# Performance work log

Measured on AMD Instinct MI355X. Metric: run time of the kernel, lower is better.

## Reference

```python
import jax, jax.numpy as jnp
import numpy as np

N_NODES = 50000
N_EDGES = 1600000
D = 128
LEAKY_SLOPE = 0.01  # torch nn.LeakyReLU default


def setup_inputs() -> dict:
    key = jax.random.key(0)
    ks = jax.random.split(key, 7)
    entity_embed = jax.random.normal(ks[0], (N_NODES, D), dtype=jnp.float32)
    W1 = jax.random.normal(ks[1], (D, D), dtype=jnp.float32) * 0.05
    b1 = jax.random.normal(ks[2], (D,), dtype=jnp.float32) * 0.05
    W2 = jax.random.normal(ks[3], (D, D), dtype=jnp.float32) * 0.05
    b2 = jax.random.normal(ks[4], (D,), dtype=jnp.float32) * 0.05
    src = jax.random.randint(ks[5], (N_EDGES,), 0, N_NODES, dtype=jnp.int32)
    dst = jax.random.randint(ks[6], (N_EDGES,), 0, N_NODES, dtype=jnp.int32)
    return {"entity_embed": entity_embed, "W1": W1, "b1": b1,
            "W2": W2, "b2": b2, "src": src, "dst": dst}


def reference(entity_embed, W1, b1, W2, b2, src, dst):
    # DGL update_all(copy_u('node','side'), sum('side','H')):
    # H[v] = sum over edges (u -> v) of entity_embed[u]
    n = entity_embed.shape[0]
    H = jax.ops.segment_sum(entity_embed[src], dst, num_segments=n)  # [N, D]
    # neighbors branch: LeakyReLU(W_1 @ H)
    neighbors = jax.nn.leaky_relu(H @ W1.T + b1, negative_slope=LEAKY_SLOPE)
    # interactions branch: LeakyReLU(W_2 @ (node * H))
    interactions = jax.nn.leaky_relu((entity_embed * H) @ W2.T + b2,
                                     negative_slope=LEAKY_SLOPE)
    # dropout is identity at inference
    return neighbors + interactions
```

## Files before the change

### kernel.cpp

```cpp
#include <hip/hip_runtime.h>

#define NN 50000
#define DD 128
#define SLOPE 0.01f
#define NB 782
#define BCAP 2560
#define ECH 6144
#define BST 512
#define PB 2
#define OVCAP 8192
#define HP 136

using bf16x8 = __attribute__((ext_vector_type(8))) short;
using f32x4  = __attribute__((ext_vector_type(4))) float;

__device__ inline float bflo(unsigned int w) { return __uint_as_float(w << 16); }
__device__ inline float bfhi(unsigned int w) { return __uint_as_float(w & 0xffff0000u); }
__device__ inline float sbf(short s) {
    return __uint_as_float(((unsigned int)(unsigned short)s) << 16);
}
__device__ inline unsigned int rnebf(float f) {
    unsigned int u = __float_as_uint(f);
    return (u + 0x7fffu + ((u >> 16) & 1u)) >> 16;
}
__device__ inline unsigned int pack2(float lo, float hi) {
    return rnebf(lo) | (rnebf(hi) << 16);
}

__global__ __launch_bounds__(BST) void count_convert(
    const float* __restrict__ E, const float* __restrict__ W1,
    const float* __restrict__ W2, const int* __restrict__ dst,
    unsigned short* __restrict__ Ebf, unsigned short* __restrict__ W1b,
    unsigned short* __restrict__ W2b, int* __restrict__ cnt_g,
    int n_edges, int nbin)
{
    const int tid = threadIdx.x;

    if (blockIdx.x >= nbin) {
        const int NE8 = NN * DD / 8;
        const int NW8 = DD * DD / 8;
        int t = (blockIdx.x - nbin) * BST + tid;
        const float* s; unsigned short* d; int idx;
        if (t < NE8)                { s = E;  d = Ebf; idx = t; }
        else if (t < NE8 + NW8)     { s = W1; d = W1b; idx = t - NE8; }
        else if (t < NE8 + 2 * NW8) { s = W2; d = W2b; idx = t - NE8 - NW8; }
        else return;
        float4 a = ((const float4*)s)[(size_t)idx * 2];
        float4 b = ((const float4*)s)[(size_t)idx * 2 + 1];
        uint4 o;
        o.x = pack2(a.x, a.y); o.y = pack2(a.z, a.w);
        o.z = pack2(b.x, b.y); o.w = pack2(b.z, b.w);
        ((uint4*)d)[idx] = o;
        return;
    }

    __shared__ int cnt[NB];
    const int e0 = blockIdx.x * ECH;
    const int m = min(ECH, n_edges - e0);

    for (int b = tid; b < NB; b += BST) cnt[b] = 0;
    __syncthreads();
    for (int i = tid; i < m; i += BST)
        atomicAdd(&cnt[dst[e0 + i] >> 6], 1);
    __syncthreads();
    for (int b = tid; b < NB; b += BST)
        cnt_g[(size_t)b * nbin + blockIdx.x] = cnt[b];
}

__global__ __launch_bounds__(256) void scan_counts(
    int* __restrict__ cnt_g, int* __restrict__ gtail,
    int* __restrict__ ovf_cnt, int nbin)
{
    if (blockIdx.x == 0 && threadIdx.x == 0) *ovf_cnt = 0;
    const int w = threadIdx.x >> 6, lane = threadIdx.x & 63;
    const int bb = blockIdx.x * 4 + w;
    if (bb >= NB) return;
    int* row = cnt_g + (size_t)bb * nbin;
    int carry = 0;
    for (int base = 0; base < nbin; base += 64) {
        int blk = base + lane;
        int v = (blk < nbin) ? row[blk] : 0;
        int incl = v;
        #pragma unroll
        for (int d = 1; d < 64; d <<= 1) {
            int t = __shfl_up(incl, d);
            if (lane >= d) incl += t;
        }
        if (blk < nbin) row[blk] = carry + incl - v;
        carry += __shfl(incl, 63);
    }
    if (lane == 0) gtail[bb] = carry;
}

__global__ __launch_bounds__(BST) void scatter_edges(
    const int* __restrict__ src, const int* __restrict__ dst,
    const int* __restrict__ cnt_g, unsigned int* __restrict__ stag,
    int* __restrict__ ovf_cnt, int2* __restrict__ ovf,
    int n_edges, int nbin)
{
    __shared__ unsigned int srt[ECH];
    __shared__ int cnt[NB], off[NB], pos[NB], gbase[NB];
    __shared__ int wsum[BST / 64];

    const int tid = threadIdx.x;
    const int e0 = blockIdx.x * ECH;
    const int m = min(ECH, n_edges - e0);

    for (int b = tid; b < NB; b += BST) cnt[b] = 0;
    __syncthreads();

    for (int i = tid; i < m; i += BST)
        atomicAdd(&cnt[dst[e0 + i] >> 6], 1);
    for (int b = tid; b < NB; b += BST)
        gbase[b] = cnt_g[(size_t)b * nbin + blockIdx.x];
    __syncthreads();

    const int lane = tid & 63, w = tid >> 6;
    int b0 = tid * PB;
    int loc[PB]; int s = 0;
    #pragma unroll
    for (int j = 0; j < PB; ++j) {
        int bb = b0 + j;
        int cv = (bb < NB) ? cnt[bb] : 0;
        loc[j] = s; s += cv;
    }
    int incl = s;
    #pragma unroll
    for (int d = 1; d < 64; d <<= 1) {
        int t2 = __shfl_up(incl, d);
        if (lane >= d) incl += t2;
    }
    if (lane == 63) wsum[w] = incl;
    __syncthreads();
    int wbase = 0;
    for (int w2 = 0; w2 < w; ++w2) wbase += wsum[w2];
    int base = wbase + incl - s;
    #pragma unroll
    for (int j = 0; j < PB; ++j) {
        int bb = b0 + j;
        if (bb < NB) { off[bb] = base + loc[j]; pos[bb] = base + loc[j]; }
    }
    __syncthreads();

    for (int i = tid; i < m; i += BST) {
        int v = dst[e0 + i];
        int u = src[e0 + i];
        int bb = v >> 6;
        int p = atomicAdd(&pos[bb], 1);
        srt[p] = (unsigned int)u | ((unsigned int)(v & 63) << 16)
               | ((unsigned int)bb << 22);
    }
    __syncthreads();

    for (int i = tid; i < m; i += BST) {
        unsigned int r = srt[i];
        int bb = (int)(r >> 22);
        int gp = gbase[bb] + (i - off[bb]);
        if (gp < BCAP) {
            stag[(size_t)bb * BCAP + gp] = r & 0x3fffffu;
        } else {
            int oi = atomicAdd(ovf_cnt, 1);
            if (oi < OVCAP)
                ovf[oi] = make_int2((int)(r & 0xffffu),
                                    bb * 64 + (int)((r >> 16) & 63));
        }
    }
}

__global__ __launch_bounds__(256, 4) void bucket_fused(
    const unsigned short* __restrict__ Ebf, const int* __restrict__ gtail,
    const unsigned int* __restrict__ stag, const int* __restrict__ ovf_cnt,
    const int2* __restrict__ ovf,
    const unsigned short* __restrict__ W1b, const unsigned short* __restrict__ W2b,
    const float* __restrict__ b1, const float* __restrict__ b2,
    float* __restrict__ out)
{
    __shared__ unsigned short sorted[BCAP];
    __shared__ unsigned short Hs[64][HP];
    __shared__ int cnt[64], off[65], pos[64];
    __shared__ int s_novf;

    const int b = blockIdx.x;
    const int tid = threadIdx.x;
    const int wave = tid >> 6;
    const int lane = tid & 63;
    int len = gtail[b]; len = len < BCAP ? len : BCAP;
    const unsigned int* seg = stag + (size_t)b * BCAP;

    if (tid == 0) { int t = *ovf_cnt; s_novf = t < OVCAP ? t : OVCAP; }
    if (tid < 64) cnt[tid] = 0;
    __syncthreads();
    for (int i = tid; i < len; i += 256)
        atomicAdd(&cnt[(seg[i] >> 16) & 63], 1);
    __syncthreads();
    if (tid < 64) {
        int cv = cnt[tid];
        int incl = cv;
        #pragma unroll
        for (int d = 1; d < 64; d <<= 1) {
            int t2 = __shfl_up(incl, d);
            if (tid >= d) incl += t2;
        }
        off[tid] = incl - cv;
        pos[tid] = incl - cv;
        if (tid == 63) off[64] = incl;
    }
    __syncthreads();
    for (int i = tid; i < len; i += 256) {
        unsigned int r = seg[i];
        int p = atomicAdd(&pos[(r >> 16) & 63], 1);
        sorted[p] = (unsigned short)(r & 0xffffu);
    }
    __syncthreads();
    const int novf = s_novf;

    const unsigned int* E1 = (const unsigned int*)Ebf;
    for (int s16 = 0; s16 < 16; ++s16) {
        const int nl = wave * 16 + s16;
        const int v = b * 64 + nl;
        if (v >= NN) break;
        float a0 = 0.f, a1 = 0.f;
        int i = off[nl], e1 = off[nl + 1];
        unsigned int r[16];
        for (; i + 16 <= e1; i += 16) {
            #pragma unroll
            for (int k = 0; k < 16; ++k)
                r[k] = E1[(size_t)sorted[i + k] * 64 + lane];
            __builtin_amdgcn_sched_barrier(0);
            #pragma unroll
            for (int k = 0; k < 16; ++k) { a0 += bflo(r[k]); a1 += bfhi(r[k]); }
        }
        for (; i + 4 <= e1; i += 4) {
            #pragma unroll
            for (int k = 0; k < 4; ++k)
                r[k] = E1[(size_t)sorted[i + k] * 64 + lane];
            __builtin_amdgcn_sched_barrier(0);
            #pragma unroll
            for (int k = 0; k < 4; ++k) { a0 += bflo(r[k]); a1 += bfhi(r[k]); }
        }
        for (; i < e1; ++i) {
            unsigned int r0 = E1[(size_t)sorted[i] * 64 + lane];
            a0 += bflo(r0); a1 += bfhi(r0);
        }
        if (novf > 0) {
            for (int k = 0; k < novf; ++k) {
                int2 e = ovf[k];
                if (e.y == v) {
                    unsigned int r0 = E1[(size_t)e.x * 64 + lane];
                    a0 += bflo(r0); a1 += bfhi(r0);
                }
            }
        }
        *(unsigned int*)&Hs[nl][lane * 2] = pack2(a0, a1);
    }

    const int v0 = b * 64 + wave * 16;
    if (v0 >= NN) return;
    const int m = lane & 15;
    const int quad = lane >> 4;

    bf16x8 aH[4], aE[4];
    const unsigned short* hrow = &Hs[wave * 16 + m][quad * 8];
    const unsigned short* erow = Ebf + (size_t)(v0 + m) * DD + quad * 8;
    #pragma unroll
    for (int ks = 0; ks < 4; ++ks) {
        bf16x8 h8 = *(const bf16x8*)(hrow + ks * 32);
        bf16x8 e8 = *(const bf16x8*)(erow + ks * 32);
        aH[ks] = h8;
        bf16x8 eh;
        #pragma unroll
        for (int j = 0; j < 8; ++j)
            eh[j] = (short)rnebf(sbf(h8[j]) * sbf(e8[j]));
        aE[ks] = eh;
    }

    #pragma unroll
    for (int jt = 0; jt < 8; ++jt) {
        const int j0 = jt * 16;
        const unsigned short* w1r = W1b + (size_t)(j0 + m) * DD + quad * 8;
        const unsigned short* w2r = W2b + (size_t)(j0 + m) * DD + quad * 8;
        f32x4 acc1 = {0.f, 0.f, 0.f, 0.f}, acc2 = {0.f, 0.f, 0.f, 0.f};
        #pragma unroll
        for (int ks = 0; ks < 4; ++ks) {
            bf16x8 bw1 = *(const bf16x8*)(w1r + ks * 32);
            bf16x8 bw2 = *(const bf16x8*)(w2r + ks * 32);
            acc1 = __builtin_amdgcn_mfma_f32_16x16x32_bf16(aH[ks], bw1, acc1, 0, 0, 0);
            acc2 = __builtin_amdgcn_mfma_f32_16x16x32_bf16(aE[ks], bw2, acc2, 0, 0, 0);
        }
        const float bb1 = b1[j0 + m], bb2 = b2[j0 + m];
        #pragma unroll
        for (int i = 0; i < 4; ++i) {
            int row = v0 + quad * 4 + i;
            if (row < NN) {
                float x1 = acc1[i] + bb1; x1 = x1 > 0.f ? x1 : SLOPE * x1;
                float x2 = acc2[i] + bb2; x2 = x2 > 0.f ? x2 : SLOPE * x2;
                out[(size_t)row * DD + j0 + m] = x1 + x2;
            }
        }
    }
}

__global__ __launch_bounds__(256) void scatter_add(
    const float* __restrict__ E, const int* __restrict__ src,
    const int* __restrict__ dst, float* __restrict__ H, int n_edges)
{
    int t = blockIdx.x * 256 + threadIdx.x;
    int e = t >> 5;
    if (e >= n_edges) return;
    int c = t & 31;
    float4 a = ((const float4*)E)[(size_t)src[e] * 32 + c];
    float* hp = H + (size_t)dst[e] * DD + c * 4;
    atomicAdd(hp + 0, a.x); atomicAdd(hp + 1, a.y);
    atomicAdd(hp + 2, a.z); atomicAdd(hp + 3, a.w);
}

__global__ __launch_bounds__(256) void fused_mlp(
    const float* __restrict__ E, const float* __restrict__ H,
    const float* __restrict__ W1, const float* __restrict__ b1,
    const float* __restrict__ W2, const float* __restrict__ b2,
    float* __restrict__ out)
{
    __shared__ float Hsf[32][DD];
    __shared__ float EHs[32][DD];
    __shared__ float W1s[DD][20];
    __shared__ float W2s[DD][20];
    const int tid = threadIdx.x;
    const int v0 = blockIdx.x * 32;
    const int nvalid = min(32, NN - v0);
    for (int i = 0; i < 4; ++i) {
        int f = tid + 256 * i;
        int n = f >> 5, c = f & 31;
        float4 h = make_float4(0.f, 0.f, 0.f, 0.f);
        float4 eh = h;
        if (n < nvalid) {
            h = ((const float4*)H)[(size_t)(v0 + n) * 32 + c];
            float4 e4 = ((const float4*)E)[(size_t)(v0 + n) * 32 + c];
            eh = make_float4(e4.x * h.x, e4.y * h.y, e4.z * h.z, e4.w * h.w);
        }
        *((float4*)&Hsf[n][c * 4]) = h;
        *((float4*)&EHs[n][c * 4]) = eh;
    }
    const int jg = tid & 63;
    const int n0 = (tid >> 6) * 8;
    float acc1a[8] = {}, acc1b[8] = {}, acc2a[8] = {}, acc2b[8] = {};
    for (int t8 = 0; t8 < 8; ++t8) {
        const int k0 = t8 * 16;
        __syncthreads();
        for (int i = 0; i < 8; ++i) {
            int f = tid + 256 * i;
            int j = f >> 4, kk = f & 15;
            W1s[j][kk] = W1[j * DD + k0 + kk];
            W2s[j][kk] = W2[j * DD + k0 + kk];
        }
        __syncthreads();
        for (int c = 0; c < 4; ++c) {
            float4 w1a = *((const float4*)&W1s[jg][c * 4]);
            float4 w1b = *((const float4*)&W1s[jg + 64][c * 4]);
            float4 w2a = *((const float4*)&W2s[jg][c * 4]);
            float4 w2b = *((const float4*)&W2s[jg + 64][c * 4]);
            const int kk = k0 + c * 4;
            for (int n = 0; n < 8; ++n) {
                float4 h = *((const float4*)&Hsf[n0 + n][kk]);
                float4 eh = *((const float4*)&EHs[n0 + n][kk]);
                acc1a[n] += h.x * w1a.x + h.y * w1a.y + h.z * w1a.z + h.w * w1a.w;
                acc1b[n] += h.x * w1b.x + h.y * w1b.y + h.z * w1b.z + h.w * w1b.w;
                acc2a[n] += eh.x * w2a.x + eh.y * w2a.y + eh.z * w2a.z + eh.w * w2a.w;
                acc2b[n] += eh.x * w2b.x + eh.y * w2b.y + eh.z * w2b.z + eh.w * w2b.w;
            }
        }
    }
    const float b1a = b1[jg], b1b = b1[jg + 64];
    const float b2a = b2[jg], b2b = b2[jg + 64];
    for (int n = 0; n < 8; ++n) {
        if (n0 + n < nvalid) {
            const int v = v0 + n0 + n;
            float x1 = acc1a[n] + b1a; x1 = x1 > 0.f ? x1 : SLOPE * x1;
            float x2 = acc2a[n] + b2a; x2 = x2 > 0.f ? x2 : SLOPE * x2;
            out[(size_t)v * DD + jg] = x1 + x2;
            float y1 = acc1b[n] + b1b; y1 = y1 > 0.f ? y1 : SLOPE * y1;
            float y2 = acc2b[n] + b2b; y2 = y2 > 0.f ? y2 : SLOPE * y2;
            out[(size_t)v * DD + jg + 64] = y1 + y2;
        }
    }
}

extern "C" void kernel_launch(void* const* d_in, const int* in_sizes, int n_in,
                              void* d_out, int out_size, void* d_ws, size_t ws_size,
                              hipStream_t stream)
{
    const float* E  = (const float*)d_in[0];
    const float* W1 = (const float*)d_in[1];
    const float* b1 = (const float*)d_in[2];
    const float* W2 = (const float*)d_in[3];
    const float* b2 = (const float*)d_in[4];
    const int* src  = (const int*)d_in[5];
    const int* dst  = (const int*)d_in[6];
    float* out = (float*)d_out;
    const int n_edges = in_sizes[5];

    char* ws = (char*)d_ws;
    auto al = [](size_t x) { return (x + 255) & ~(size_t)255; };

    const int nbin = (n_edges + ECH - 1) / ECH;

    const size_t off_tail = 0;
    const size_t off_ovfc = (size_t)NB * 4;
    const size_t off_ovf  = al(off_ovfc + 4);
    const size_t off_stag = al(off_ovf + (size_t)OVCAP * 8);
    const size_t off_Ebf  = al(off_stag + (size_t)NB * BCAP * 4);
    const size_t off_W1b  = al(off_Ebf + (size_t)NN * DD * 2);
    const size_t off_W2b  = al(off_W1b + (size_t)DD * DD * 2);
    const size_t off_cntg = al(off_W2b + (size_t)DD * DD * 2);
    const size_t need_bf  = off_cntg + (size_t)NB * nbin * 4;

    if (ws_size >= need_bf) {
        int*  gtail   = (int*)(ws + off_tail);
        int*  ovf_cnt = (int*)(ws + off_ovfc);
        int2* ovf     = (int2*)(ws + off_ovf);
        unsigned int*   stag = (unsigned int*)(ws + off_stag);
        unsigned short* Ebf  = (unsigned short*)(ws + off_Ebf);
        unsigned short* W1b  = (unsigned short*)(ws + off_W1b);
        unsigned short* W2b  = (unsigned short*)(ws + off_W2b);
        int*  cnt_g   = (int*)(ws + off_cntg);

        const int ncv  = NN * DD / 8 + 2 * (DD * DD / 8);
        const int ncvb = (ncv + BST - 1) / BST;

        count_convert<<<nbin + ncvb, BST, 0, stream>>>(
            E, W1, W2, dst, Ebf, W1b, W2b, cnt_g, n_edges, nbin);
        scan_counts<<<(NB + 3) / 4, 256, 0, stream>>>(
            cnt_g, gtail, ovf_cnt, nbin);
        scatter_edges<<<nbin, BST, 0, stream>>>(
            src, dst, cnt_g, stag, ovf_cnt, ovf, n_edges, nbin);
        bucket_fused<<<NB, 256, 0, stream>>>(
            Ebf, gtail, stag, ovf_cnt, ovf, W1b, W2b, b1, b2, out);
        return;
    }

    const size_t hbytes = (size_t)NN * DD * sizeof(float);
    float* H = (ws_size >= hbytes) ? (float*)ws : out;
    hipMemsetAsync(H, 0, hbytes, stream);
    scatter_add<<<((n_edges * 32) + 255) / 256, 256, 0, stream>>>(
        E, src, dst, H, n_edges);
    fused_mlp<<<(NN + 31) / 32, 256, 0, stream>>>(E, H, W1, b1, W2, b2, out);
}
```

Baseline: 196.8 us.

## Fuse binning passes into a cooperative kernel and quarter-split bf16 embedding layout

Merges the count/convert, scan, and scatter kernels into one cooperative-launch kernel that uses grid syncs, with the old three-kernel path kept as a fallback if the cooperative launch fails. The bf16 embedding copy is stored as four 32-column slabs so the gather phase reads 64-byte rows per quarter, letting each wave accumulate four destination nodes at once. The edge chunk size and bucket capacity shrink so the chunk count fits a cooperative grid. The aim is to remove launch gaps and improve gather locality. The costs are grid-sync overhead, more overflow-list traffic from the smaller bucket capacity, and four separate passes over the edge list per node.

```diff
diff --git a/kernel.cpp b/kernel.cpp
--- a/kernel.cpp
+++ b/kernel.cpp
@@ -1,11 +1,13 @@
 #include <hip/hip_runtime.h>
+#include <hip/hip_cooperative_groups.h>
+namespace cg = cooperative_groups;
 
 #define NN 50000
 #define DD 128
 #define SLOPE 0.01f
 #define NB 782
-#define BCAP 2560
-#define ECH 6144
+#define BCAP 2304
+#define ECH 3072
 #define BST 512
 #define PB 2
 #define OVCAP 8192
@@ -27,93 +29,100 @@
     return rnebf(lo) | (rnebf(hi) << 16);
 }
 
-__global__ __launch_bounds__(BST) void count_convert(
+__device__ inline void convert_item(
     const float* __restrict__ E, const float* __restrict__ W1,
-    const float* __restrict__ W2, const int* __restrict__ dst,
-    unsigned short* __restrict__ Ebf, unsigned short* __restrict__ W1b,
-    unsigned short* __restrict__ W2b, int* __restrict__ cnt_g,
-    int n_edges, int nbin)
-{
-    const int tid = threadIdx.x;
-
-    if (blockIdx.x >= nbin) {
-        const int NE8 = NN * DD / 8;
-        const int NW8 = DD * DD / 8;
-        int t = (blockIdx.x - nbin) * BST + tid;
-        const float* s; unsigned short* d; int idx;
-        if (t < NE8)                { s = E;  d = Ebf; idx = t; }
-        else if (t < NE8 + NW8)     { s = W1; d = W1b; idx = t - NE8; }
-        else if (t < NE8 + 2 * NW8) { s = W2; d = W2b; idx = t - NE8 - NW8; }
-        else return;
-        float4 a = ((const float4*)s)[(size_t)idx * 2];
-        float4 b = ((const float4*)s)[(size_t)idx * 2 + 1];
+    const float* __restrict__ W2, unsigned short* __restrict__ Ebf,
+    unsigned short* __restrict__ W1b, unsigned short* __restrict__ W2b, int t)
+{
+    const int NE8 = NN * DD / 8;
+    const int NW8 = DD * DD / 8;
+    const float* s; unsigned short* d; size_t oidx;
+    if (t < NE8) {
+        s = E;
+        int r = t >> 4, sl = t & 15;
+        int p = sl >> 2, q4 = sl & 3;
+        oidx = ((size_t)p * NN + r) * 4 + q4;
+        d = Ebf;
+        float4 a = ((const float4*)s)[(size_t)t * 2];
+        float4 b = ((const float4*)s)[(size_t)t * 2 + 1];
         uint4 o;
         o.x = pack2(a.x, a.y); o.y = pack2(a.z, a.w);
         o.z = pack2(b.x, b.y); o.w = pack2(b.z, b.w);
-        ((uint4*)d)[idx] = o;
+        ((uint4*)d)[oidx] = o;
         return;
     }
-
-    __shared__ int cnt[NB];
-    const int e0 = blockIdx.x * ECH;
-    const int m = min(ECH, n_edges - e0);
-
-    for (int b = tid; b < NB; b += BST) cnt[b] = 0;
-    __syncthreads();
-    for (int i = tid; i < m; i += BST)
-        atomicAdd(&cnt[dst[e0 + i] >> 6], 1);
-    __syncthreads();
-    for (int b = tid; b < NB; b += BST)
-        cnt_g[(size_t)b * nbin + blockIdx.x] = cnt[b];
-}
-
-__global__ __launch_bounds__(256) void scan_counts(
+    int idx;
+    if (t < NE8 + NW8)          { s = W1; d = W1b; idx = t - NE8; }
+    else if (t < NE8 + 2 * NW8) { s = W2; d = W2b; idx = t - NE8 - NW8; }
+    else return;
+    float4 a = ((const float4*)s)[(size_t)idx * 2];
+    float4 b = ((const float4*)s)[(size_t)idx * 2 + 1];
+    uint4 o;
+    o.x = pack2(a.x, a.y); o.y = pack2(a.z, a.w);
+    o.z = pack2(b.x, b.y); o.w = pack2(b.z, b.w);
+    ((uint4*)d)[idx] = o;
+}
+
+__global__ __launch_bounds__(BST) void bin_coop(
+    const float* __restrict__ E, const float* __restrict__ W1,
+    const float* __restrict__ W2, const int* __restrict__ src,
+    const int* __restrict__ dst, unsigned short* __restrict__ Ebf,
+    unsigned short* __restrict__ W1b, unsigned short* __restrict__ W2b,
     int* __restrict__ cnt_g, int* __restrict__ gtail,
-    int* __restrict__ ovf_cnt, int nbin)
-{
-    if (blockIdx.x == 0 && threadIdx.x == 0) *ovf_cnt = 0;
-    const int w = threadIdx.x >> 6, lane = threadIdx.x & 63;
-    const int bb = blockIdx.x * 4 + w;
-    if (bb >= NB) return;
-    int* row = cnt_g + (size_t)bb * nbin;
-    int carry = 0;
-    for (int base = 0; base < nbin; base += 64) {
-        int blk = base + lane;
-        int v = (blk < nbin) ? row[blk] : 0;
-        int incl = v;
-        #pragma unroll
-        for (int d = 1; d < 64; d <<= 1) {
-            int t = __shfl_up(incl, d);
-            if (lane >= d) incl += t;
-        }
-        if (blk < nbin) row[blk] = carry + incl - v;
-        carry += __shfl(incl, 63);
-    }
-    if (lane == 0) gtail[bb] = carry;
-}
-
-__global__ __launch_bounds__(BST) void scatter_edges(
-    const int* __restrict__ src, const int* __restrict__ dst,
-    const int* __restrict__ cnt_g, unsigned int* __restrict__ stag,
-    int* __restrict__ ovf_cnt, int2* __restrict__ ovf,
-    int n_edges, int nbin)
+    unsigned int* __restrict__ stag, int* __restrict__ ovf_cnt,
+    int2* __restrict__ ovf, int n_edges, int nchunk)
 {
     __shared__ unsigned int srt[ECH];
     __shared__ int cnt[NB], off[NB], pos[NB], gbase[NB];
     __shared__ int wsum[BST / 64];
 
     const int tid = threadIdx.x;
-    const int e0 = blockIdx.x * ECH;
+    const int blk = blockIdx.x;
+    const int e0 = blk * ECH;
     const int m = min(ECH, n_edges - e0);
 
     for (int b = tid; b < NB; b += BST) cnt[b] = 0;
     __syncthreads();
-
     for (int i = tid; i < m; i += BST)
         atomicAdd(&cnt[dst[e0 + i] >> 6], 1);
+    __syncthreads();
     for (int b = tid; b < NB; b += BST)
-        gbase[b] = cnt_g[(size_t)b * nbin + blockIdx.x];
-    __syncthreads();
+        cnt_g[(size_t)b * nchunk + blk] = cnt[b];
+
+    const int NCV = NN * DD / 8 + 2 * (DD * DD / 8);
+    for (int t = blk * BST + tid; t < NCV; t += gridDim.x * BST)
+        convert_item(E, W1, W2, Ebf, W1b, W2b, t);
+
+    __threadfence();
+    cg::this_grid().sync();
+
+    {
+        const int gw = blk * (BST / 64) + (tid >> 6);
+        const int lane = tid & 63;
+        if (gw == 0 && lane == 0) *ovf_cnt = 0;
+        if (gw < NB) {
+            int* row = cnt_g + (size_t)gw * nchunk;
+            int carry = 0;
+            for (int base = 0; base < nchunk; base += 64) {
+                int c = base + lane;
+                int v = (c < nchunk) ? row[c] : 0;
+                int incl = v;
+                #pragma unroll
+                for (int d = 1; d < 64; d <<= 1) {
+                    int t2 = __shfl_up(incl, d);
+                    if (lane >= d) incl += t2;
+                }
+                if (c < nchunk) row[c] = carry + incl - v;
+                carry += __shfl(incl, 63);
+            }
+            if (lane == 0) gtail[gw] = carry;
+        }
+    }
+    __threadfence();
+    cg::this_grid().sync();
+
+    for (int b = tid; b < NB; b += BST)
+        gbase[b] = cnt_g[(size_t)b * nchunk + blk];
 
     const int lane = tid & 63, w = tid >> 6;
     int b0 = tid * PB;
@@ -167,6 +176,130 @@
     }
 }
 
+__global__ __launch_bounds__(BST) void count_convert(
+    const float* __restrict__ E, const float* __restrict__ W1,
+    const float* __restrict__ W2, const int* __restrict__ dst,
+    unsigned short* __restrict__ Ebf, unsigned short* __restrict__ W1b,
+    unsigned short* __restrict__ W2b, int* __restrict__ cnt_g,
+    int n_edges, int nchunk)
+{
+    const int tid = threadIdx.x;
+    if (blockIdx.x >= nchunk) {
+        int t = (blockIdx.x - nchunk) * BST + tid;
+        convert_item(E, W1, W2, Ebf, W1b, W2b, t);
+        return;
+    }
+    __shared__ int cnt[NB];
+    const int e0 = blockIdx.x * ECH;
+    const int m = min(ECH, n_edges - e0);
+    for (int b = tid; b < NB; b += BST) cnt[b] = 0;
+    __syncthreads();
+    for (int i = tid; i < m; i += BST)
+        atomicAdd(&cnt[dst[e0 + i] >> 6], 1);
+    __syncthreads();
+    for (int b = tid; b < NB; b += BST)
+        cnt_g[(size_t)b * nchunk + blockIdx.x] = cnt[b];
+}
+
+__global__ __launch_bounds__(256) void scan_counts(
+    int* __restrict__ cnt_g, int* __restrict__ gtail,
+    int* __restrict__ ovf_cnt, int nchunk)
+{
+    if (blockIdx.x == 0 && threadIdx.x == 0) *ovf_cnt = 0;
+    const int w = threadIdx.x >> 6, lane = threadIdx.x & 63;
+    const int bb = blockIdx.x * 4 + w;
+    if (bb >= NB) return;
+    int* row = cnt_g + (size_t)bb * nchunk;
+    int carry = 0;
+    for (int base = 0; base < nchunk; base += 64) {
+        int blk = base + lane;
+        int v = (blk < nchunk) ? row[blk] : 0;
+        int incl = v;
+        #pragma unroll
+        for (int d = 1; d < 64; d <<= 1) {
+            int t = __shfl_up(incl, d);
+            if (lane >= d) incl += t;
+        }
+        if (blk < nchunk) row[blk] = carry + incl - v;
+        carry += __shfl(incl, 63);
+    }
+    if (lane == 0) gtail[bb] = carry;
+}
+
+__global__ __launch_bounds__(BST) void scatter_edges(
+    const int* __restrict__ src, const int* __restrict__ dst,
+    const int* __restrict__ cnt_g, unsigned int* __restrict__ stag,
+    int* __restrict__ ovf_cnt, int2* __restrict__ ovf,
+    int n_edges, int nchunk)
+{
+    __shared__ unsigned int srt[ECH];
+    __shared__ int cnt[NB], off[NB], pos[NB], gbase[NB];
+    __shared__ int wsum[BST / 64];
+
+    const int tid = threadIdx.x;
+    const int e0 = blockIdx.x * ECH;
+    const int m = min(ECH, n_edges - e0);
+
+    for (int b = tid; b < NB; b += BST) cnt[b] = 0;
+    __syncthreads();
+    for (int i = tid; i < m; i += BST)
+        atomicAdd(&cnt[dst[e0 + i] >> 6], 1);
+    for (int b = tid; b < NB; b += BST)
+        gbase[b] = cnt_g[(size_t)b * nchunk + blockIdx.x];
+    __syncthreads();
+
+    const int lane = tid & 63, w = tid >> 6;
+    int b0 = tid * PB;
+    int loc[PB]; int s = 0;
+    #pragma unroll
+    for (int j = 0; j < PB; ++j) {
+        int bb = b0 + j;
+        int cv = (bb < NB) ? cnt[bb] : 0;
+        loc[j] = s; s += cv;
+    }
+    int incl = s;
+    #pragma unroll
+    for (int d = 1; d < 64; d <<= 1) {
+        int t2 = __shfl_up(incl, d);
+        if (lane >= d) incl += t2;
+    }
+    if (lane == 63) wsum[w] = incl;
+    __syncthreads();
+    int wbase = 0;
+    for (int w2 = 0; w2 < w; ++w2) wbase += wsum[w2];
+    int base = wbase + incl - s;
+    #pragma unroll
+    for (int j = 0; j < PB; ++j) {
+        int bb = b0 + j;
+        if (bb < NB) { off[bb] = base + loc[j]; pos[bb] = base + loc[j]; }
+    }
+    __syncthreads();
+
+    for (int i = tid; i < m; i += BST) {
+        int v = dst[e0 + i];
+        int u = src[e0 + i];
+        int bb = v >> 6;
+        int p = atomicAdd(&pos[bb], 1);
+        srt[p] = (unsigned int)u | ((unsigned int)(v & 63) << 16)
+               | ((unsigned int)bb << 22);
+    }
+    __syncthreads();
+
+    for (int i = tid; i < m; i += BST) {
+        unsigned int r = srt[i];
+        int bb = (int)(r >> 22);
+        int gp = gbase[bb] + (i - off[bb]);
+        if (gp < BCAP) {
+            stag[(size_t)bb * BCAP + gp] = r & 0x3fffffu;
+        } else {
+            int oi = atomicAdd(ovf_cnt, 1);
+            if (oi < OVCAP)
+                ovf[oi] = make_int2((int)(r & 0xffffu),
+                                    bb * 64 + (int)((r >> 16) & 63));
+        }
+    }
+}
+
 __global__ __launch_bounds__(256, 4) void bucket_fused(
     const unsigned short* __restrict__ Ebf, const int* __restrict__ gtail,
     const unsigned int* __restrict__ stag, const int* __restrict__ ovf_cnt,
@@ -214,44 +347,48 @@
     __syncthreads();
     const int novf = s_novf;
 
-    const unsigned int* E1 = (const unsigned int*)Ebf;
-    for (int s16 = 0; s16 < 16; ++s16) {
-        const int nl = wave * 16 + s16;
-        const int v = b * 64 + nl;
-        if (v >= NN) break;
-        float a0 = 0.f, a1 = 0.f;
-        int i = off[nl], e1 = off[nl + 1];
-        unsigned int r[16];
-        for (; i + 16 <= e1; i += 16) {
-            #pragma unroll
-            for (int k = 0; k < 16; ++k)
-                r[k] = E1[(size_t)sorted[i + k] * 64 + lane];
-            __builtin_amdgcn_sched_barrier(0);
-            #pragma unroll
-            for (int k = 0; k < 16; ++k) { a0 += bflo(r[k]); a1 += bfhi(r[k]); }
-        }
-        for (; i + 4 <= e1; i += 4) {
-            #pragma unroll
-            for (int k = 0; k < 4; ++k)
-                r[k] = E1[(size_t)sorted[i + k] * 64 + lane];
-            __builtin_amdgcn_sched_barrier(0);
-            #pragma unroll
-            for (int k = 0; k < 4; ++k) { a0 += bflo(r[k]); a1 += bfhi(r[k]); }
-        }
-        for (; i < e1; ++i) {
-            unsigned int r0 = E1[(size_t)sorted[i] * 64 + lane];
-            a0 += bflo(r0); a1 += bfhi(r0);
-        }
-        if (novf > 0) {
-            for (int k = 0; k < novf; ++k) {
-                int2 e = ovf[k];
-                if (e.y == v) {
-                    unsigned int r0 = E1[(size_t)e.x * 64 + lane];
-                    a0 += bflo(r0); a1 += bfhi(r0);
+    const int c = lane & 15;
+    const int g2 = lane >> 4;
+    for (int q = 0; q < 4; ++q) {
+        const unsigned int* Eq = (const unsigned int*)Ebf + (size_t)q * NN * 16;
+        for (int s4 = 0; s4 < 4; ++s4) {
+            const int nl = wave * 16 + s4 * 4 + g2;
+            const int v = b * 64 + nl;
+            if (v >= NN) continue;
+            float a0 = 0.f, a1 = 0.f;
+            int i = off[nl], e1v = off[nl + 1];
+            unsigned int r[16];
+            for (; i + 16 <= e1v; i += 16) {
+                #pragma unroll
+                for (int k = 0; k < 16; ++k)
+                    r[k] = Eq[(size_t)sorted[i + k] * 16 + c];
+                __builtin_amdgcn_sched_barrier(0);
+                #pragma unroll
+                for (int k = 0; k < 16; ++k) { a0 += bflo(r[k]); a1 += bfhi(r[k]); }
+            }
+            for (; i + 4 <= e1v; i += 4) {
+                #pragma unroll
+                for (int k = 0; k < 4; ++k)
+                    r[k] = Eq[(size_t)sorted[i + k] * 16 + c];
+                __builtin_amdgcn_sched_barrier(0);
+                #pragma unroll
+                for (int k = 0; k < 4; ++k) { a0 += bflo(r[k]); a1 += bfhi(r[k]); }
+            }
+            for (; i < e1v; ++i) {
+                unsigned int r0 = Eq[(size_t)sorted[i] * 16 + c];
+                a0 += bflo(r0); a1 += bfhi(r0);
+            }
+            if (novf > 0) {
+                for (int k = 0; k < novf; ++k) {
+                    int2 e = ovf[k];
+                    if (e.y == v) {
+                        unsigned int r0 = Eq[(size_t)e.x * 16 + c];
+                        a0 += bflo(r0); a1 += bfhi(r0);
+                    }
                 }
             }
-        }
-        *(unsigned int*)&Hs[nl][lane * 2] = pack2(a0, a1);
+            *(unsigned int*)&Hs[nl][(q * 16 + c) * 2] = pack2(a0, a1);
+        }
     }
 
     const int v0 = b * 64 + wave * 16;
@@ -261,11 +398,11 @@
 
     bf16x8 aH[4], aE[4];
     const unsigned short* hrow = &Hs[wave * 16 + m][quad * 8];
-    const unsigned short* erow = Ebf + (size_t)(v0 + m) * DD + quad * 8;
     #pragma unroll
     for (int ks = 0; ks < 4; ++ks) {
         bf16x8 h8 = *(const bf16x8*)(hrow + ks * 32);
-        bf16x8 e8 = *(const bf16x8*)(erow + ks * 32);
+        bf16x8 e8 = *(const bf16x8*)(Ebf + (size_t)ks * NN * 32
+                                         + (size_t)(v0 + m) * 32 + quad * 8);
         aH[ks] = h8;
         bf16x8 eh;
         #pragma unroll
@@ -401,7 +538,7 @@
     char* ws = (char*)d_ws;
     auto al = [](size_t x) { return (x + 255) & ~(size_t)255; };
 
-    const int nbin = (n_edges + ECH - 1) / ECH;
+    const int nchunk = (n_edges + ECH - 1) / ECH;
 
     const size_t off_tail = 0;
     const size_t off_ovfc = (size_t)NB * 4;
@@ -411,7 +548,7 @@
     const size_t off_W1b  = al(off_Ebf + (size_t)NN * DD * 2);
     const size_t off_W2b  = al(off_W1b + (size_t)DD * DD * 2);
     const size_t off_cntg = al(off_W2b + (size_t)DD * DD * 2);
-    const size_t need_bf  = off_cntg + (size_t)NB * nbin * 4;
+    const size_t need_bf  = off_cntg + (size_t)NB * nchunk * 4;
 
     if (ws_size >= need_bf) {
         int*  gtail   = (int*)(ws + off_tail);
@@ -423,15 +560,25 @@
         unsigned short* W2b  = (unsigned short*)(ws + off_W2b);
         int*  cnt_g   = (int*)(ws + off_cntg);
 
-        const int ncv  = NN * DD / 8 + 2 * (DD * DD / 8);
-        const int ncvb = (ncv + BST - 1) / BST;
-
-        count_convert<<<nbin + ncvb, BST, 0, stream>>>(
-            E, W1, W2, dst, Ebf, W1b, W2b, cnt_g, n_edges, nbin);
-        scan_counts<<<(NB + 3) / 4, 256, 0, stream>>>(
-            cnt_g, gtail, ovf_cnt, nbin);
-        scatter_edges<<<nbin, BST, 0, stream>>>(
-            src, dst, cnt_g, stag, ovf_cnt, ovf, n_edges, nbin);
+        int ne = n_edges, nc = nchunk;
+        void* kargs[] = {
+            (void*)&E, (void*)&W1, (void*)&W2, (void*)&src, (void*)&dst,
+            (void*)&Ebf, (void*)&W1b, (void*)&W2b, (void*)&cnt_g,
+            (void*)&gtail, (void*)&stag, (void*)&ovf_cnt, (void*)&ovf,
+            (void*)&ne, (void*)&nc };
+        hipError_t cerr = hipLaunchCooperativeKernel(
+            (const void*)bin_coop, dim3(nchunk), dim3(BST), kargs, 0, stream);
+        if (cerr != hipSuccess) {
+            (void)hipGetLastError();
+            const int NCV = NN * DD / 8 + 2 * (DD * DD / 8);
+            const int ncvb = (NCV + BST - 1) / BST;
+            count_convert<<<nchunk + ncvb, BST, 0, stream>>>(
+                E, W1, W2, dst, Ebf, W1b, W2b, cnt_g, n_edges, nchunk);
+            scan_counts<<<(NB + 3) / 4, 256, 0, stream>>>(
+                cnt_g, gtail, ovf_cnt, nchunk);
+            scatter_edges<<<nchunk, BST, 0, stream>>>(
+                src, dst, cnt_g, stag, ovf_cnt, ovf, n_edges, nchunk);
+        }
         bucket_fused<<<NB, 256, 0, stream>>>(
             Ebf, gtail, stag, ovf_cnt, ovf, W1b, W2b, b1, b2, out);
         return;
```

Result: slower. 523.4 us (+165.9%).
